# Optimization experiments

Hardware: AMD Instinct MI355X
Metric: run time of the kernel (lower is better)

The kernel has to match this reference:

```python
import jax, jax.numpy as jnp
import numpy as np

H = 4096
W = 4096
N_BOXES = 200000


def gaussian_mount() -> jnp.ndarray:
    # 3x3 gaussian, sigma=1, normalized so max == 1 (matches gaussian_2d + /max)
    y, x = np.ogrid[-1:2, -1:2]
    g = np.exp(-(x * x + y * y) / 2.0)
    g[g < np.finfo(g.dtype).eps * g.max()] = 0
    g = g / g.max()
    return jnp.asarray(g, dtype=jnp.float32)


def setup_inputs() -> dict:
    key = jax.random.key(0)
    boxes = jax.random.uniform(key, (N_BOXES, 4), dtype=jnp.float32)  # cx,cy,w,h in [0,1)
    return {"boxes": boxes, "mount": gaussian_mount(), "w": W, "h": H}


def reference(boxes, mount, w, h):
    # centers in pixel coords (floor via int cast, same as .long())
    cx = (boxes[:, 0] * w).astype(jnp.int32)  # [B]
    cy = (boxes[:, 1] * h).astype(jnp.int32)  # [B]

    sizemap = jnp.zeros((2, h, w), dtype=jnp.float32).at[:, cy, cx].set(boxes[:, 2:4].T)

    # A 3x3 mount is stamped only when the full window fits inside the image
    # (the torch loop's slice produces a too-small target otherwise and skips).
    valid = (cx >= 1) & (cx <= w - 2) & (cy >= 1) & (cy <= h - 2)  # [B]

    off = jnp.arange(-1, 2)
    rows = jnp.clip(cy, 1, h - 2)[:, None, None] + off[:, None]  # [B,3,3] (clip keeps idx in-range)
    cols = jnp.clip(cx, 1, w - 2)[:, None, None] + off[None, :]  # [B,3,3]
    vals = jnp.where(valid[:, None, None], mount[None, :, :], 0.0)  # invalid -> 0, max no-op

    # order-independent scatter-max (sequential torch.max loop is equivalent)
    heat = jnp.zeros((h, w), dtype=jnp.float32).at[rows, cols].max(vals)

    heatmap = heat[None, None]      # [1,1,h,w]
    sizemap = sizemap[None]         # [1,2,h,w]
    return heatmap, sizemap
```

## Files before the change

kernel.cpp:

```cpp
#include <hip/hip_runtime.h>
#include <hip/hip_bf16.h>

#define IMG_H 4096
#define IMG_W 4096
#define NPIX (IMG_H * IMG_W)

#define TILE 64
#define TILES_X (IMG_W / TILE)
#define TILES_Y (IMG_H / TILE)
#define NBINS (TILES_X * TILES_Y)
#define BIN_CAP 256

__global__ __launch_bounds__(256) void bin_boxes_kernel(
    const float* __restrict__ boxes,
    int* __restrict__ counts,
    int* __restrict__ bins,
    int nboxes)
{
    int b = blockIdx.x * blockDim.x + threadIdx.x;
    if (b >= nboxes) return;
    float4 bx = reinterpret_cast<const float4*>(boxes)[b];
    int cx = (int)(bx.x * (float)IMG_W);
    int cy = (int)(bx.y * (float)IMG_H);
    int valid = (cx >= 1 && cx <= IMG_W - 2 && cy >= 1 && cy <= IMG_H - 2) ? 1 : 0;
    int pack = b | ((cx & 63) << 18) | ((cy & 63) << 24) | (valid << 30);
    int bin = (cy >> 6) * TILES_X + (cx >> 6);
    int slot = atomicAdd(&counts[bin], 1);
    if (slot < BIN_CAP) bins[bin * BIN_CAP + slot] = pack;
}

__global__ __launch_bounds__(256) void tile_kernel(
    const float* __restrict__ boxes,
    const float* __restrict__ mount,
    const int* __restrict__ counts,
    const int* __restrict__ bins,
    float* __restrict__ heat,
    float* __restrict__ s0,
    float* __restrict__ s1)
{
    __shared__ int lidx[TILE * TILE];
    __shared__ unsigned int bm[TILE + 2][4];
    __shared__ int pfx[10];
    __shared__ int bbase[9];

    int tid = threadIdx.x;
    int tile = blockIdx.x;
    int tx = tile & (TILES_X - 1);
    int ty = tile >> 6;

    for (int i = tid; i < TILE * TILE; i += 256) lidx[i] = -1;
    for (int i = tid; i < (TILE + 2) * 4; i += 256) ((unsigned int*)bm)[i] = 0u;

    if (tid < 9) {
        int nty = ty + tid / 3 - 1;
        int ntx = tx + tid % 3 - 1;
        int cnt = 0, base = 0;
        if ((unsigned)nty < TILES_Y && (unsigned)ntx < TILES_X) {
            int bin = nty * TILES_X + ntx;
            cnt = min(counts[bin], BIN_CAP);
            base = bin * BIN_CAP;
        }
        pfx[tid + 1] = cnt;
        bbase[tid] = base;
        if (tid == 0) pfx[0] = 0;
    }
    __syncthreads();
    if (tid == 0) {
#pragma unroll
        for (int j = 0; j < 9; ++j) pfx[j + 1] += pfx[j];
    }
    __syncthreads();
    int S = pfx[9];

    for (int i = tid; i < S; i += 256) {
        int j = 0;
        while (pfx[j + 1] <= i) ++j;
        int p = bins[bbase[j] + (i - pfx[j])];
        int lx = (p >> 18) & 63;
        int ly = (p >> 24) & 63;
        if (j == 4) atomicMax(&lidx[ly * TILE + lx], p);
        if (p & (1 << 30)) {
            int Lx = lx + (j % 3) * 64 - 64;
            int Ly = ly + (j / 3) * 64 - 64;
            if (Lx >= -1 && Lx <= TILE && Ly >= -1 && Ly <= TILE) {
                int pos = Lx + 1;
                atomicOr(&bm[Ly + 1][pos >> 5], 1u << (pos & 31));
            }
        }
    }
    __syncthreads();

    float mvC = mount[4];
    float mvE = mount[1];
    float mvK = mount[0];
    int ty0 = ty * TILE, tx0 = tx * TILE;

#pragma unroll
    for (int pass = 0; pass < 4; ++pass) {
        int idx = pass * 1024 + tid * 4;
        int r = idx >> 6;
        int xb = idx & 63;

        uint4 w0 = *(const uint4*)&bm[r][0];
        uint4 w1 = *(const uint4*)&bm[r + 1][0];
        uint4 w2 = *(const uint4*)&bm[r + 2][0];
        unsigned long long V0 = ((unsigned long long)w0.y << 32) | w0.x;
        unsigned long long V1 = ((unsigned long long)w1.y << 32) | w1.x;
        unsigned long long V2 = ((unsigned long long)w2.y << 32) | w2.x;
        if (xb) {
            V0 = (V0 >> xb) | ((unsigned long long)w0.z << (64 - xb));
            V1 = (V1 >> xb) | ((unsigned long long)w1.z << (64 - xb));
            V2 = (V2 >> xb) | ((unsigned long long)w2.z << (64 - xb));
        }
        unsigned int C = (unsigned int)(V1 >> 1);
        unsigned int E = (unsigned int)V1 | (unsigned int)(V1 >> 2)
                       | (unsigned int)(V0 >> 1) | (unsigned int)(V2 >> 1);
        unsigned int K = (unsigned int)V0 | (unsigned int)(V0 >> 2)
                       | (unsigned int)V2 | (unsigned int)(V2 >> 2);

        float h[4];
#pragma unroll
        for (int jj = 0; jj < 4; ++jj) {
            float v = 0.f;
            if ((K >> jj) & 1) v = mvK;
            if ((E >> jj) & 1) v = mvE;
            if ((C >> jj) & 1) v = mvC;
            h[jj] = v;
        }

        int g = (ty0 + r) * IMG_W + tx0 + xb;
        *reinterpret_cast<float4*>(&heat[g]) = make_float4(h[0], h[1], h[2], h[3]);

        int4 iv = *reinterpret_cast<const int4*>(&lidx[idx]);
        float4 ow = make_float4(0.f, 0.f, 0.f, 0.f);
        float4 oh = make_float4(0.f, 0.f, 0.f, 0.f);
        if (iv.x >= 0) { float4 bb = reinterpret_cast<const float4*>(boxes)[iv.x & 0x3FFFF]; ow.x = bb.z; oh.x = bb.w; }
        if (iv.y >= 0) { float4 bb = reinterpret_cast<const float4*>(boxes)[iv.y & 0x3FFFF]; ow.y = bb.z; oh.y = bb.w; }
        if (iv.z >= 0) { float4 bb = reinterpret_cast<const float4*>(boxes)[iv.z & 0x3FFFF]; ow.z = bb.z; oh.z = bb.w; }
        if (iv.w >= 0) { float4 bb = reinterpret_cast<const float4*>(boxes)[iv.w & 0x3FFFF]; ow.w = bb.z; oh.w = bb.w; }
        *reinterpret_cast<float4*>(&s0[g]) = ow;
        *reinterpret_cast<float4*>(&s1[g]) = oh;
    }
}

extern "C" void kernel_launch(void* const* d_in, const int* in_sizes, int n_in,
                              void* d_out, int out_size, void* d_ws, size_t ws_size,
                              hipStream_t stream) {
    const float* boxes = (const float*)d_in[0];
    const float* mount = (const float*)d_in[1];
    int nboxes = in_sizes[0] / 4;

    float* out  = (float*)d_out;
    float* heat = out;
    float* s0   = out + NPIX;
    float* s1   = out + 2 * NPIX;

    int* counts = (int*)d_ws;
    int* bins   = counts + NBINS;

    hipMemsetAsync(counts, 0, NBINS * sizeof(int), stream);

    int bgrid = (nboxes + 255) / 256;
    bin_boxes_kernel<<<bgrid, 256, 0, stream>>>(boxes, counts, bins, nboxes);

    tile_kernel<<<NBINS, 256, 0, stream>>>(boxes, mount, counts, bins, heat, s0, s1);
}
```

Baseline: 220.4 us.

## Bin box sizes alongside metadata and use nontemporal output stores

The binning kernel now writes each box's width and height into a parallel bin array, so the tile kernel no longer gathers from the full boxes array per occupied pixel. The winning box per pixel writes its w into shared memory for the s0 pass, then its h for a separate s1 pass. All output stores become nontemporal vector stores to avoid polluting cache with write-only data. This adds workspace traffic, extra barriers and a second sweep over the tile.

```diff
diff --git a/kernel.cpp b/kernel.cpp
--- a/kernel.cpp
+++ b/kernel.cpp
@@ -11,10 +11,19 @@
 #define NBINS (TILES_X * TILES_Y)
 #define BIN_CAP 256
 
+typedef float f4v __attribute__((ext_vector_type(4)));
+
+static __device__ __forceinline__ void nt_store4(float* p, float a, float b,
+                                                 float c, float d) {
+    f4v v = {a, b, c, d};
+    __builtin_nontemporal_store(v, (f4v*)p);
+}
+
 __global__ __launch_bounds__(256) void bin_boxes_kernel(
     const float* __restrict__ boxes,
     int* __restrict__ counts,
-    int* __restrict__ bins,
+    int* __restrict__ bins_meta,
+    float2* __restrict__ bins_wh,
     int nboxes)
 {
     int b = blockIdx.x * blockDim.x + threadIdx.x;
@@ -26,14 +35,17 @@
     int pack = b | ((cx & 63) << 18) | ((cy & 63) << 24) | (valid << 30);
     int bin = (cy >> 6) * TILES_X + (cx >> 6);
     int slot = atomicAdd(&counts[bin], 1);
-    if (slot < BIN_CAP) bins[bin * BIN_CAP + slot] = pack;
+    if (slot < BIN_CAP) {
+        bins_meta[bin * BIN_CAP + slot] = pack;
+        bins_wh[bin * BIN_CAP + slot] = make_float2(bx.z, bx.w);
+    }
 }
 
 __global__ __launch_bounds__(256) void tile_kernel(
-    const float* __restrict__ boxes,
     const float* __restrict__ mount,
     const int* __restrict__ counts,
-    const int* __restrict__ bins,
+    const int* __restrict__ bins_meta,
+    const float2* __restrict__ bins_wh,
     float* __restrict__ heat,
     float* __restrict__ s0,
     float* __restrict__ s1)
@@ -75,7 +87,7 @@
     for (int i = tid; i < S; i += 256) {
         int j = 0;
         while (pfx[j + 1] <= i) ++j;
-        int p = bins[bbase[j] + (i - pfx[j])];
+        int p = bins_meta[bbase[j] + (i - pfx[j])];
         int lx = (p >> 18) & 63;
         int ly = (p >> 24) & 63;
         if (j == 4) atomicMax(&lidx[ly * TILE + lx], p);
@@ -90,6 +102,20 @@
     }
     __syncthreads();
 
+    int cnt4 = pfx[5] - pfx[4];
+    bool match = false;
+    int mypx = 0;
+    float2 mywh = make_float2(0.f, 0.f);
+    if (tid < cnt4) {
+        int m = bins_meta[bbase[4] + tid];
+        mywh = bins_wh[bbase[4] + tid];
+        mypx = ((m >> 24) & 63) * TILE + ((m >> 18) & 63);
+        match = (lidx[mypx] == m);
+    }
+    __syncthreads();
+    if (match) lidx[mypx] = __float_as_int(mywh.x);
+    __syncthreads();
+
     float mvC = mount[4];
     float mvE = mount[1];
     float mvK = mount[0];
@@ -129,17 +155,32 @@
         }
 
         int g = (ty0 + r) * IMG_W + tx0 + xb;
-        *reinterpret_cast<float4*>(&heat[g]) = make_float4(h[0], h[1], h[2], h[3]);
+        nt_store4(&heat[g], h[0], h[1], h[2], h[3]);
 
         int4 iv = *reinterpret_cast<const int4*>(&lidx[idx]);
-        float4 ow = make_float4(0.f, 0.f, 0.f, 0.f);
-        float4 oh = make_float4(0.f, 0.f, 0.f, 0.f);
-        if (iv.x >= 0) { float4 bb = reinterpret_cast<const float4*>(boxes)[iv.x & 0x3FFFF]; ow.x = bb.z; oh.x = bb.w; }
-        if (iv.y >= 0) { float4 bb = reinterpret_cast<const float4*>(boxes)[iv.y & 0x3FFFF]; ow.y = bb.z; oh.y = bb.w; }
-        if (iv.z >= 0) { float4 bb = reinterpret_cast<const float4*>(boxes)[iv.z & 0x3FFFF]; ow.z = bb.z; oh.z = bb.w; }
-        if (iv.w >= 0) { float4 bb = reinterpret_cast<const float4*>(boxes)[iv.w & 0x3FFFF]; ow.w = bb.z; oh.w = bb.w; }
-        *reinterpret_cast<float4*>(&s0[g]) = ow;
-        *reinterpret_cast<float4*>(&s1[g]) = oh;
+        nt_store4(&s0[g],
+                  iv.x >= 0 ? __int_as_float(iv.x) : 0.f,
+                  iv.y >= 0 ? __int_as_float(iv.y) : 0.f,
+                  iv.z >= 0 ? __int_as_float(iv.z) : 0.f,
+                  iv.w >= 0 ? __int_as_float(iv.w) : 0.f);
+    }
+    __syncthreads();
+
+    if (match) lidx[mypx] = __float_as_int(mywh.y);
+    __syncthreads();
+
+#pragma unroll
+    for (int pass = 0; pass < 4; ++pass) {
+        int idx = pass * 1024 + tid * 4;
+        int r = idx >> 6;
+        int xb = idx & 63;
+        int g = (ty0 + r) * IMG_W + tx0 + xb;
+        int4 iv = *reinterpret_cast<const int4*>(&lidx[idx]);
+        nt_store4(&s1[g],
+                  iv.x >= 0 ? __int_as_float(iv.x) : 0.f,
+                  iv.y >= 0 ? __int_as_float(iv.y) : 0.f,
+                  iv.z >= 0 ? __int_as_float(iv.z) : 0.f,
+                  iv.w >= 0 ? __int_as_float(iv.w) : 0.f);
     }
 }
 
@@ -155,13 +196,16 @@
     float* s0   = out + NPIX;
     float* s1   = out + 2 * NPIX;
 
-    int* counts = (int*)d_ws;
-    int* bins   = counts + NBINS;
+    int*    counts    = (int*)d_ws;
+    int*    bins_meta = counts + NBINS;
+    float2* bins_wh   = (float2*)(bins_meta + NBINS * BIN_CAP);
 
     hipMemsetAsync(counts, 0, NBINS * sizeof(int), stream);
 
     int bgrid = (nboxes + 255) / 256;
-    bin_boxes_kernel<<<bgrid, 256, 0, stream>>>(boxes, counts, bins, nboxes);
-
-    tile_kernel<<<NBINS, 256, 0, stream>>>(boxes, mount, counts, bins, heat, s0, s1);
-}
+    bin_boxes_kernel<<<bgrid, 256, 0, stream>>>(boxes, counts, bins_meta,
+                                                bins_wh, nboxes);
+
+    tile_kernel<<<NBINS, 256, 0, stream>>>(mount, counts, bins_meta, bins_wh,
+                                           heat, s0, s1);
+}
```

After: 234.5 us. +6.4%, slower.

## Store box sizes in bins and compute neighbor prefix sums per thread

Applied to the files above, without the earlier changes.

The binning kernel now writes each box's width and height next to its packed metadata in a bin-local array. The tile kernel looks up sizes through a bin-local slot index instead of gathering randomly from the global boxes array. Each thread also computes the 9-neighbor counts and prefix sums in registers, which removes the shared prefix arrays and one barrier. In exchange the binning kernel does an extra scattered write per box, and every thread performs nine global count loads instead of nine threads doing them once.

```diff
diff --git a/kernel.cpp b/kernel.cpp
--- a/kernel.cpp
+++ b/kernel.cpp
@@ -14,7 +14,8 @@
 __global__ __launch_bounds__(256) void bin_boxes_kernel(
     const float* __restrict__ boxes,
     int* __restrict__ counts,
-    int* __restrict__ bins,
+    int* __restrict__ bins_meta,
+    float2* __restrict__ bins_wh,
     int nboxes)
 {
     int b = blockIdx.x * blockDim.x + threadIdx.x;
@@ -26,22 +27,23 @@
     int pack = b | ((cx & 63) << 18) | ((cy & 63) << 24) | (valid << 30);
     int bin = (cy >> 6) * TILES_X + (cx >> 6);
     int slot = atomicAdd(&counts[bin], 1);
-    if (slot < BIN_CAP) bins[bin * BIN_CAP + slot] = pack;
+    if (slot < BIN_CAP) {
+        bins_meta[bin * BIN_CAP + slot] = pack;
+        bins_wh[bin * BIN_CAP + slot] = make_float2(bx.z, bx.w);
+    }
 }
 
 __global__ __launch_bounds__(256) void tile_kernel(
-    const float* __restrict__ boxes,
     const float* __restrict__ mount,
     const int* __restrict__ counts,
-    const int* __restrict__ bins,
+    const int* __restrict__ bins_meta,
+    const float2* __restrict__ bins_wh,
     float* __restrict__ heat,
     float* __restrict__ s0,
     float* __restrict__ s1)
 {
     __shared__ int lidx[TILE * TILE];
     __shared__ unsigned int bm[TILE + 2][4];
-    __shared__ int pfx[10];
-    __shared__ int bbase[9];
 
     int tid = threadIdx.x;
     int tile = blockIdx.x;
@@ -51,34 +53,34 @@
     for (int i = tid; i < TILE * TILE; i += 256) lidx[i] = -1;
     for (int i = tid; i < (TILE + 2) * 4; i += 256) ((unsigned int*)bm)[i] = 0u;
 
-    if (tid < 9) {
-        int nty = ty + tid / 3 - 1;
-        int ntx = tx + tid % 3 - 1;
-        int cnt = 0, base = 0;
-        if ((unsigned)nty < TILES_Y && (unsigned)ntx < TILES_X) {
-            int bin = nty * TILES_X + ntx;
-            cnt = min(counts[bin], BIN_CAP);
-            base = bin * BIN_CAP;
-        }
-        pfx[tid + 1] = cnt;
-        bbase[tid] = base;
-        if (tid == 0) pfx[0] = 0;
+    int cnt[9], base[9];
+#pragma unroll
+    for (int j = 0; j < 9; ++j) {
+        int nty = ty + j / 3 - 1;
+        int ntx = tx + j % 3 - 1;
+        bool ok = ((unsigned)nty < TILES_Y) & ((unsigned)ntx < TILES_X);
+        int bin = nty * TILES_X + ntx;
+        base[j] = bin * BIN_CAP;
+        cnt[j] = ok ? min(counts[bin], BIN_CAP) : 0;
     }
+    int pfx[10];
+    pfx[0] = 0;
+#pragma unroll
+    for (int j = 0; j < 9; ++j) pfx[j + 1] = pfx[j] + cnt[j];
+    int S = pfx[9];
     __syncthreads();
-    if (tid == 0) {
-#pragma unroll
-        for (int j = 0; j < 9; ++j) pfx[j + 1] += pfx[j];
-    }
-    __syncthreads();
-    int S = pfx[9];
 
     for (int i = tid; i < S; i += 256) {
         int j = 0;
-        while (pfx[j + 1] <= i) ++j;
-        int p = bins[bbase[j] + (i - pfx[j])];
+#pragma unroll
+        for (int k = 1; k < 9; ++k) j += (i >= pfx[k]);
+        int rel = i - pfx[j];
+        int p = bins_meta[base[j] + rel];
         int lx = (p >> 18) & 63;
         int ly = (p >> 24) & 63;
-        if (j == 4) atomicMax(&lidx[ly * TILE + lx], p);
+        if (j == 4) {
+            atomicMax(&lidx[ly * TILE + lx], ((p & 0x3FFFF) << 8) | rel);
+        }
         if (p & (1 << 30)) {
             int Lx = lx + (j % 3) * 64 - 64;
             int Ly = ly + (j / 3) * 64 - 64;
@@ -94,6 +96,7 @@
     float mvE = mount[1];
     float mvK = mount[0];
     int ty0 = ty * TILE, tx0 = tx * TILE;
+    const float2* mywh = &bins_wh[tile * BIN_CAP];
 
 #pragma unroll
     for (int pass = 0; pass < 4; ++pass) {
@@ -131,13 +134,13 @@
         int g = (ty0 + r) * IMG_W + tx0 + xb;
         *reinterpret_cast<float4*>(&heat[g]) = make_float4(h[0], h[1], h[2], h[3]);
 
-        int4 iv = *reinterpret_cast<const int4*>(&lidx[idx]);
+        int4 iw = *reinterpret_cast<const int4*>(&lidx[idx]);
         float4 ow = make_float4(0.f, 0.f, 0.f, 0.f);
         float4 oh = make_float4(0.f, 0.f, 0.f, 0.f);
-        if (iv.x >= 0) { float4 bb = reinterpret_cast<const float4*>(boxes)[iv.x & 0x3FFFF]; ow.x = bb.z; oh.x = bb.w; }
-        if (iv.y >= 0) { float4 bb = reinterpret_cast<const float4*>(boxes)[iv.y & 0x3FFFF]; ow.y = bb.z; oh.y = bb.w; }
-        if (iv.z >= 0) { float4 bb = reinterpret_cast<const float4*>(boxes)[iv.z & 0x3FFFF]; ow.z = bb.z; oh.z = bb.w; }
-        if (iv.w >= 0) { float4 bb = reinterpret_cast<const float4*>(boxes)[iv.w & 0x3FFFF]; ow.w = bb.z; oh.w = bb.w; }
+        if (iw.x >= 0) { float2 wh = mywh[iw.x & 255]; ow.x = wh.x; oh.x = wh.y; }
+        if (iw.y >= 0) { float2 wh = mywh[iw.y & 255]; ow.y = wh.x; oh.y = wh.y; }
+        if (iw.z >= 0) { float2 wh = mywh[iw.z & 255]; ow.z = wh.x; oh.z = wh.y; }
+        if (iw.w >= 0) { float2 wh = mywh[iw.w & 255]; ow.w = wh.x; oh.w = wh.y; }
         *reinterpret_cast<float4*>(&s0[g]) = ow;
         *reinterpret_cast<float4*>(&s1[g]) = oh;
     }
@@ -155,13 +158,16 @@
     float* s0   = out + NPIX;
     float* s1   = out + 2 * NPIX;
 
-    int* counts = (int*)d_ws;
-    int* bins   = counts + NBINS;
+    int*    counts    = (int*)d_ws;
+    int*    bins_meta = counts + NBINS;
+    float2* bins_wh   = (float2*)(bins_meta + NBINS * BIN_CAP);
 
     hipMemsetAsync(counts, 0, NBINS * sizeof(int), stream);
 
     int bgrid = (nboxes + 255) / 256;
-    bin_boxes_kernel<<<bgrid, 256, 0, stream>>>(boxes, counts, bins, nboxes);
+    bin_boxes_kernel<<<bgrid, 256, 0, stream>>>(boxes, counts, bins_meta,
+                                                bins_wh, nboxes);
 
-    tile_kernel<<<NBINS, 256, 0, stream>>>(boxes, mount, counts, bins, heat, s0, s1);
+    tile_kernel<<<NBINS, 256, 0, stream>>>(mount, counts, bins_meta, bins_wh,
+                                           heat, s0, s1);
 }
```

Measured after the change: 223.1 us. No clear change (+1.2%).

## Push halo entries into neighbor bins and embed box sizes in bin records

Applied to the files above, without the earlier changes.

The binning kernel now writes 16-byte bin records that carry the box width and height. For valid boxes on a tile edge it also writes extra halo records into the adjacent bins. Each tile kernel then reads only its own bin, instead of scanning nine neighbor bins through a prefix walk and gathering box sizes from the global boxes array. The cost is wider bin writes, extra atomics for edge boxes, and a larger workspace (bins are four times bigger), which may exceed the available scratch space.

```diff
diff --git a/kernel.cpp b/kernel.cpp
--- a/kernel.cpp
+++ b/kernel.cpp
@@ -14,7 +14,7 @@
 __global__ __launch_bounds__(256) void bin_boxes_kernel(
     const float* __restrict__ boxes,
     int* __restrict__ counts,
-    int* __restrict__ bins,
+    int4* __restrict__ bins4,
     int nboxes)
 {
     int b = blockIdx.x * blockDim.x + threadIdx.x;
@@ -22,26 +22,49 @@
     float4 bx = reinterpret_cast<const float4*>(boxes)[b];
     int cx = (int)(bx.x * (float)IMG_W);
     int cy = (int)(bx.y * (float)IMG_H);
+    int lx = cx & 63, ly = cy & 63;
+    int tx = cx >> 6, ty = cy >> 6;
     int valid = (cx >= 1 && cx <= IMG_W - 2 && cy >= 1 && cy <= IMG_H - 2) ? 1 : 0;
-    int pack = b | ((cx & 63) << 18) | ((cy & 63) << 24) | (valid << 30);
-    int bin = (cy >> 6) * TILES_X + (cx >> 6);
+
+    int meta = b | (lx << 18) | (ly << 24) | (valid << 30);
+    int bin = ty * TILES_X + tx;
     int slot = atomicAdd(&counts[bin], 1);
-    if (slot < BIN_CAP) bins[bin * BIN_CAP + slot] = pack;
+    if (slot < BIN_CAP)
+        bins4[bin * BIN_CAP + slot] =
+            make_int4(meta, __float_as_int(bx.z), __float_as_int(bx.w), 0);
+
+    if (valid) {
+        int dx = (lx == 0) ? -1 : (lx == 63 ? 1 : 0);
+        int dy = (ly == 0) ? -1 : (ly == 63 ? 1 : 0);
+        if (dx | dy) {
+#pragma unroll
+            for (int k = 0; k < 3; ++k) {
+                int rdx = (k == 0 || k == 2) ? dx : 0;
+                int rdy = (k == 1 || k == 2) ? dy : 0;
+                if ((k == 0 && dx == 0) || (k == 1 && dy == 0) ||
+                    (k == 2 && (dx == 0 || dy == 0))) continue;
+                int nbin = (ty + rdy) * TILES_X + (tx + rdx);
+                int lxp = lx - 64 * rdx + 1;
+                int lyp = ly - 64 * rdy + 1;
+                int rmeta = 0x80000000 | lxp | (lyp << 7);
+                int rslot = atomicAdd(&counts[nbin], 1);
+                if (rslot < BIN_CAP)
+                    bins4[nbin * BIN_CAP + rslot] = make_int4(rmeta, 0, 0, 0);
+            }
+        }
+    }
 }
 
 __global__ __launch_bounds__(256) void tile_kernel(
-    const float* __restrict__ boxes,
     const float* __restrict__ mount,
     const int* __restrict__ counts,
-    const int* __restrict__ bins,
+    const int4* __restrict__ bins4,
     float* __restrict__ heat,
     float* __restrict__ s0,
     float* __restrict__ s1)
 {
     __shared__ int lidx[TILE * TILE];
     __shared__ unsigned int bm[TILE + 2][4];
-    __shared__ int pfx[10];
-    __shared__ int bbase[9];
 
     int tid = threadIdx.x;
     int tile = blockIdx.x;
@@ -51,41 +74,24 @@
     for (int i = tid; i < TILE * TILE; i += 256) lidx[i] = -1;
     for (int i = tid; i < (TILE + 2) * 4; i += 256) ((unsigned int*)bm)[i] = 0u;
 
-    if (tid < 9) {
-        int nty = ty + tid / 3 - 1;
-        int ntx = tx + tid % 3 - 1;
-        int cnt = 0, base = 0;
-        if ((unsigned)nty < TILES_Y && (unsigned)ntx < TILES_X) {
-            int bin = nty * TILES_X + ntx;
-            cnt = min(counts[bin], BIN_CAP);
-            base = bin * BIN_CAP;
-        }
-        pfx[tid + 1] = cnt;
-        bbase[tid] = base;
-        if (tid == 0) pfx[0] = 0;
-    }
+    const int4* mybin = &bins4[tile * BIN_CAP];
+    int mycnt = min(counts[tile], BIN_CAP);
     __syncthreads();
-    if (tid == 0) {
-#pragma unroll
-        for (int j = 0; j < 9; ++j) pfx[j + 1] += pfx[j];
-    }
-    __syncthreads();
-    int S = pfx[9];
 
-    for (int i = tid; i < S; i += 256) {
-        int j = 0;
-        while (pfx[j + 1] <= i) ++j;
-        int p = bins[bbase[j] + (i - pfx[j])];
-        int lx = (p >> 18) & 63;
-        int ly = (p >> 24) & 63;
-        if (j == 4) atomicMax(&lidx[ly * TILE + lx], p);
-        if (p & (1 << 30)) {
-            int Lx = lx + (j % 3) * 64 - 64;
-            int Ly = ly + (j / 3) * 64 - 64;
-            if (Lx >= -1 && Lx <= TILE && Ly >= -1 && Ly <= TILE) {
-                int pos = Lx + 1;
-                atomicOr(&bm[Ly + 1][pos >> 5], 1u << (pos & 31));
+    for (int i = tid; i < mycnt; i += 256) {
+        int p = mybin[i].x;
+        if (p >= 0) {
+            int lx = (p >> 18) & 63;
+            int ly = (p >> 24) & 63;
+            atomicMax(&lidx[ly * TILE + lx], ((p & 0x3FFFF) << 8) | i);
+            if (p & (1 << 30)) {
+                int pos = lx + 1;
+                atomicOr(&bm[ly + 1][pos >> 5], 1u << (pos & 31));
             }
+        } else {
+            int lxp = p & 127;
+            int lyp = (p >> 7) & 127;
+            atomicOr(&bm[lyp][lxp >> 5], 1u << (lxp & 31));
         }
     }
     __syncthreads();
@@ -131,13 +137,13 @@
         int g = (ty0 + r) * IMG_W + tx0 + xb;
         *reinterpret_cast<float4*>(&heat[g]) = make_float4(h[0], h[1], h[2], h[3]);
 
-        int4 iv = *reinterpret_cast<const int4*>(&lidx[idx]);
+        int4 iw = *reinterpret_cast<const int4*>(&lidx[idx]);
         float4 ow = make_float4(0.f, 0.f, 0.f, 0.f);
         float4 oh = make_float4(0.f, 0.f, 0.f, 0.f);
-        if (iv.x >= 0) { float4 bb = reinterpret_cast<const float4*>(boxes)[iv.x & 0x3FFFF]; ow.x = bb.z; oh.x = bb.w; }
-        if (iv.y >= 0) { float4 bb = reinterpret_cast<const float4*>(boxes)[iv.y & 0x3FFFF]; ow.y = bb.z; oh.y = bb.w; }
-        if (iv.z >= 0) { float4 bb = reinterpret_cast<const float4*>(boxes)[iv.z & 0x3FFFF]; ow.z = bb.z; oh.z = bb.w; }
-        if (iv.w >= 0) { float4 bb = reinterpret_cast<const float4*>(boxes)[iv.w & 0x3FFFF]; ow.w = bb.z; oh.w = bb.w; }
+        if (iw.x >= 0) { int4 e = mybin[iw.x & 255]; ow.x = __int_as_float(e.y); oh.x = __int_as_float(e.z); }
+        if (iw.y >= 0) { int4 e = mybin[iw.y & 255]; ow.y = __int_as_float(e.y); oh.y = __int_as_float(e.z); }
+        if (iw.z >= 0) { int4 e = mybin[iw.z & 255]; ow.z = __int_as_float(e.y); oh.z = __int_as_float(e.z); }
+        if (iw.w >= 0) { int4 e = mybin[iw.w & 255]; ow.w = __int_as_float(e.y); oh.w = __int_as_float(e.z); }
         *reinterpret_cast<float4*>(&s0[g]) = ow;
         *reinterpret_cast<float4*>(&s1[g]) = oh;
     }
@@ -155,13 +161,13 @@
     float* s0   = out + NPIX;
     float* s1   = out + 2 * NPIX;
 
-    int* counts = (int*)d_ws;
-    int* bins   = counts + NBINS;
+    int*  counts = (int*)d_ws;
+    int4* bins4  = (int4*)(counts + NBINS);
 
     hipMemsetAsync(counts, 0, NBINS * sizeof(int), stream);
 
     int bgrid = (nboxes + 255) / 256;
-    bin_boxes_kernel<<<bgrid, 256, 0, stream>>>(boxes, counts, bins, nboxes);
+    bin_boxes_kernel<<<bgrid, 256, 0, stream>>>(boxes, counts, bins4, nboxes);
 
-    tile_kernel<<<NBINS, 256, 0, stream>>>(boxes, mount, counts, bins, heat, s0, s1);
+    tile_kernel<<<NBINS, 256, 0, stream>>>(mount, counts, bins4, heat, s0, s1);
 }
```

New measurement: 222.2 us. No clear change (+0.8%).
